# Kernel optimization log

Hardware: AMD Instinct MI355X
Metric: run time of the kernel (lower is better)

Reference implementation:

```python
import jax, jax.numpy as jnp
from jax import lax
import numpy as np

B, T = 32, 15
THR1, THR2 = 15.0, 10.0  # conv1_t, conv2_t


def _conv(x, w):
    # x: (B,T,C,H,W) cumulative potentials/spikes; conv applied per timestep
    b, t, c, h, wd = x.shape
    y = lax.conv_general_dilated(x.reshape(b * t, c, h, wd), w, (1, 1), 'VALID',
                                 dimension_numbers=('NCHW', 'OIHW', 'NCHW'))
    return y.reshape(b, t, *y.shape[1:])


def _pool(x, k, s):
    b, t, c, h, wd = x.shape
    y = lax.reduce_window(x.reshape(b * t, c, h, wd), -jnp.inf, lax.max,
                          (1, 1, k, k), (1, 1, s, s), 'VALID')
    return y.reshape(b, t, *y.shape[1:])


def _pad(x, p):
    return jnp.pad(x, ((0, 0), (0, 0), (0, 0), (p, p), (p, p)))


def _fire(pot, thr):
    # sf.fire: F.threshold_(pot, thr, 0); spk = sign
    th = jnp.where(pot > thr, pot, 0.0)
    return jnp.sign(th), th


def _winner_class(pot, spk):
    # sf.get_k_winners(pot, kwta=1, r=0, spk): earliest spike, tie-break by potential
    b, t = spk.shape[:2]
    cnt = spk.sum(axis=1)                                   # (B,F,H,W) spike counts
    first = jnp.clip((t - cnt).astype(jnp.int32), 0, t - 1)  # earliest spike time
    vals = jnp.take_along_axis(pot, first[:, None], axis=1)[:, 0]  # pot at spike time
    trunc = spk * vals[:, None]                              # (B,T,F,H,W)
    v = trunc.reshape(b, -1).max(axis=1) * t                 # dominance offset per sample
    total = (trunc + spk * v[:, None, None, None, None]).sum(axis=1)  # (B,F,H,W)
    flat = total.reshape(b, -1)
    idx = jnp.argmax(flat, axis=1)
    mx = jnp.max(flat, axis=1)
    hw = pot.shape[-1] * pot.shape[-2]
    feat = idx // hw
    # decision_map: 10 classes x 20 features each -> class = feat // 20; -1 if no spike
    return jnp.where(mx != 0, feat // 20, -1).astype(jnp.int32)


def setup_inputs() -> dict:
    key = jax.random.key(0)
    k1, k2, k3, k4 = jax.random.split(key, 4)
    # cumulative binary spike wave: neuron fires at t_fire and stays 1 afterwards
    t_fire = jax.random.randint(k1, (B, 18, 32, 32), 0, T + 1)
    inp = (jnp.arange(T)[None, :, None, None, None] >= t_fire[:, None]).astype(jnp.float32)
    w1 = 0.8 + 0.05 * jax.random.normal(k2, (90, 18, 7, 7), dtype=jnp.float32)
    w2 = 0.8 + 0.05 * jax.random.normal(k3, (250, 90, 5, 5), dtype=jnp.float32)
    w3 = 0.8 + 0.05 * jax.random.normal(k4, (200, 250, 5, 5), dtype=jnp.float32)
    return {'input': inp, 'w1': w1, 'w2': w2, 'w3': w3, 'max_layer': 3}


def reference(input, w1, w2, w3, max_layer):
    # eval-mode forward of CIFAR10Net
    x = _pad(input, 2)                       # (B,T,18,36,36)
    spk1, pot1 = _fire(_conv(x, w1), THR1)   # (B,T,90,30,30)
    if max_layer == 1:
        return spk1, pot1
    spk2, pot2 = _fire(_conv(_pad(_pool(spk1, 2, 2), 1), w2), THR2)  # (B,T,250,13,13)
    if max_layer == 2:
        return spk2, pot2
    pot3 = _conv(_pad(_pool(spk2, 3, 3), 2), w3)   # (B,T,200,4,4)
    t = pot3.shape[1]
    mask = (jnp.arange(t) == t - 1).astype(pot3.dtype)[None, :, None, None, None]
    spk3 = jnp.sign(pot3 * mask)             # fire with threshold=None: only last step
    cls = _winner_class(pot3, spk3)          # (B,) predicted class or -1
    return cls, pot3
```

## Files before the change

kernel.cpp:

```cpp
#include <hip/hip_runtime.h>

#define NB 32
#define NT 15


__device__ __forceinline__ void tr_tile(const float* __restrict__ src, float* __restrict__ dst,
                                        int F, int K, int KK, int CIN, int nkt, int t, int tid) {
    __shared__ float lds[32][33];
    int kt = t % nkt, ft = t / nkt;
    int k0 = kt * 32, f0 = ft * 32;
    int tx = tid & 31, ty = tid >> 5;
#pragma unroll
    for (int i = 0; i < 4; i++) {
        int fl = ty + 8 * i;
        int f = f0 + fl, k = k0 + tx;
        lds[fl][tx] = (f < F && k < K) ? src[(size_t)f * K + k] : 0.f;
    }
    __syncthreads();
#pragma unroll
    for (int i = 0; i < 4; i++) {
        int row = ty + 8 * i;
        int k = k0 + row, f = f0 + tx;
        if (k < K && f < F) {
            int j = (k % KK) * CIN + k / KK;
            dst[(size_t)j * F + f] = lds[tx][row];
        }
    }
}

__global__ __launch_bounds__(256) void k_pre1(const float* __restrict__ inp,
                                              const float* __restrict__ w1,
                                              const float* __restrict__ w2,
                                              const float* __restrict__ w3,
                                              unsigned char* __restrict__ ft0,
                                              float* __restrict__ wT1, float* __restrict__ wT2,
                                              float* __restrict__ wT3,
                                              float* __restrict__ Pmin1) {
    int blk = blockIdx.x, tid = threadIdx.x;
    if (blk < 972) {
        int idx = blk * 256 + tid;
        int xx = idx % 36, rest = idx / 36;
        int yy = rest % 36; rest /= 36;
        int g = rest % 6;  int b = rest / 6;
        unsigned char* dst = ft0 + ((size_t)(b * 36 + yy) * 36 + xx) * 18 + g * 3;
        int x = xx - 2, y = yy - 2;
        if (x >= 0 && x < 32 && y >= 0 && y < 32) {
            int c0 = 0, c1 = 0, c2 = 0;
            const float* p = inp + ((size_t)b * NT * 18 + g * 3) * 1024 + y * 32 + x;
#pragma unroll
            for (int t = 0; t < NT; t++) {
                c0 += (p[(size_t)(t * 18 + 0) * 1024] != 0.f);
                c1 += (p[(size_t)(t * 18 + 1) * 1024] != 0.f);
                c2 += (p[(size_t)(t * 18 + 2) * 1024] != 0.f);
            }
            dst[0] = (unsigned char)(15 - c0);
            dst[1] = (unsigned char)(15 - c1);
            dst[2] = (unsigned char)(15 - c2);
        } else {
            dst[0] = 15; dst[1] = 15; dst[2] = 15;
        }
    } else if (blk < 2996) {
        const float* src; float* dst;
        int F, K, KK, CIN, nkt, t;
        if (blk < 1056)      { src = w1; dst = wT1; F = 90;  K = 882;  KK = 49; CIN = 18;  nkt = 28;  t = blk - 972; }
        else if (blk < 1624) { src = w2; dst = wT2; F = 250; K = 2250; KK = 25; CIN = 90;  nkt = 71;  t = blk - 1056; }
        else                 { src = w3; dst = wT3; F = 200; K = 6250; KK = 25; CIN = 250; nkt = 196; t = blk - 1624; }
        tr_tile(src, dst, F, K, KK, CIN, nkt, t, tid);
    } else if (blk == 2996) {
        if (tid < 90)  wT1[882 * 90 + tid] = 0.f;
        if (tid < 250) wT2[(size_t)2250 * 250 + tid] = 0.f;
        if (tid < 200) wT3[(size_t)6250 * 200 + tid] = 0.f;
    } else {
        int bb = blk - 2997;
        __shared__ float wm[4];
        float m = 1e30f;
#pragma unroll
        for (int k = 0; k < 8; k++) {
            int i = bb * 2048 + k * 256 + tid;
            if (i < 90 * 882) m = fminf(m, w1[i]);
        }
        for (int o = 32; o > 0; o >>= 1) m = fminf(m, __shfl_down(m, o));
        if ((tid & 63) == 0) wm[tid >> 6] = m;
        __syncthreads();
        if (tid == 0) Pmin1[bb] = fminf(fminf(wm[0], wm[1]), fminf(wm[2], wm[3]));
    }
}

__global__ __launch_bounds__(256) void k_pre2(const unsigned char* __restrict__ ft0,
                                              const float* __restrict__ wT2,
                                              const float* __restrict__ wT3,
                                              const float* __restrict__ Pmin1,
                                              unsigned char* __restrict__ zmap,
                                              float* __restrict__ PosS2, float* __restrict__ PosS3,
                                              float* __restrict__ m1) {
    int blk = blockIdx.x, tid = threadIdx.x;
    if (blk < 162) {
        int idx = blk * 256 + tid;
        const unsigned char* p = ft0 + (size_t)idx * 18;
        int z = 0;
#pragma unroll
        for (int c = 0; c < 18; c++) z += (p[c] == 0);
        zmap[idx] = (unsigned char)z;
    } else if (blk < 187) {
        int pos = blk - 162;
        int f = tid < 250 ? tid : 249;
        float acc = 0.f;
        for (int c = 0; c < 90; c++) acc += wT2[(size_t)(pos * 90 + c) * 250 + f];
        if (tid < 250) PosS2[pos * 256 + tid] = acc;
    } else if (blk < 212) {
        int pos = blk - 187;
        int f = tid < 200 ? tid : 199;
        float acc = 0.f;
        for (int c = 0; c < 250; c++) acc += wT3[(size_t)(pos * 250 + c) * 200 + f];
        if (tid < 200) PosS3[pos * 200 + tid] = acc;
    } else {
        if (tid < 64) {
            float m = (tid < 40) ? Pmin1[tid] : 1e30f;
            for (int o = 32; o > 0; o >>= 1) m = fminf(m, __shfl_down(m, o));
            if (tid == 0) m1[0] = m;
        }
    }
}

__global__ __launch_bounds__(256) void k_pre3(const float* __restrict__ PosS2,
                                              const float* __restrict__ PosS3,
                                              float* __restrict__ W2e, float* __restrict__ W3s) {
    int b = blockIdx.x, tid = threadIdx.x;
    if (b < 169) {
        int f = tid < 250 ? tid : 249;
        int oy = b / 13, ox = b - oy * 13;
        float s = 0.f;
#pragma unroll
        for (int pos = 0; pos < 25; pos++) {
            int r = pos / 5, x = pos - r * 5;
            int gy = oy + r, gx = ox + x;
            if (!(gy == 0 || gy == 16 || gx == 0 || gx == 16)) s += PosS2[pos * 256 + f];
        }
        if (tid < 250) W2e[b * 256 + tid] = s;
    } else {
        int px = b - 169;
        int f = tid < 200 ? tid : 199;
        int oy = px >> 2, ox = px & 3;
        int r0 = max(0, 2 - oy), r1 = min(4, 5 - oy);
        int x0 = max(0, 2 - ox), x1 = min(4, 5 - ox);
        float s = 0.f;
        for (int r = r0; r <= r1; r++)
            for (int x = x0; x <= x1; x++)
                s += PosS3[(r * 5 + x) * 200 + f];
        if (tid < 200) W3s[px * 200 + tid] = s;
    }
}

__global__ __launch_bounds__(128) void k_conv1f(const unsigned char* __restrict__ ft0,
                                                const unsigned char* __restrict__ zmap,
                                                const float* __restrict__ wT1,
                                                const float* __restrict__ m1p,
                                                unsigned char* __restrict__ ft1) {
    __shared__ __align__(16) int list[896];
    __shared__ int cnt, pcnt, cnt0s;
    int tid = threadIdx.x;
    int px = blockIdx.x, b = blockIdx.y;
    int oy = px / 30, ox = px - oy * 30;
    int zv = 0;
    if (tid < 49) zv = zmap[(b * 36 + oy + tid / 7) * 36 + ox + tid % 7];
    if (tid < 64) {
        for (int o = 32; o > 0; o >>= 1) zv += __shfl_down(zv, o);
        if (tid == 0) cnt0s = zv;
    }
    __syncthreads();
    if ((float)cnt0s * m1p[0] > 15.0f) {
        if (tid < 90) ft1[((size_t)(b * 30 + oy) * 30 + ox) * 90 + tid] = 0;
        return;
    }
    const unsigned char* base = ft0 + ((size_t)(b * 36 + oy) * 36 + ox) * 18;
    unsigned char myft[7];
#pragma unroll
    for (int k = 0; k < 7; k++) {
        int j = tid + k * 128;
        if (j < 882) {
            int r = j / 126;
            myft[k] = base[j + 522 * r];
        } else myft[k] = 255;
    }
    int f = tid < 90 ? tid : 89;
    const char* wb = (const char*)(wT1 + f);
    const int zoff = 882 * 90 * 4;
    float acc = 0.f; int ft = 15;
    for (int s = 0; s < 15; s++) {
        if (tid == 0) cnt = 0;
        __syncthreads();
#pragma unroll
        for (int k = 0; k < 7; k++) {
            if ((int)myft[k] == s) { int p = atomicAdd(&cnt, 1); list[p] = (tid + k * 128) * 360; }
        }
        __syncthreads();
        if (tid == 0) {
            int c0 = cnt, cp = (c0 + 7) & ~7;
            for (int i = c0; i < cp; i++) list[i] = zoff;
            pcnt = cp;
        }
        __syncthreads();
        int e = pcnt;
        for (int i = 0; i < e; i += 8) {
            int4 p0 = *(const int4*)(list + i);
            int4 p1 = *(const int4*)(list + i + 4);
            int o0 = __builtin_amdgcn_readfirstlane(p0.x);
            int o1 = __builtin_amdgcn_readfirstlane(p0.y);
            int o2 = __builtin_amdgcn_readfirstlane(p0.z);
            int o3 = __builtin_amdgcn_readfirstlane(p0.w);
            int o4 = __builtin_amdgcn_readfirstlane(p1.x);
            int o5 = __builtin_amdgcn_readfirstlane(p1.y);
            int o6 = __builtin_amdgcn_readfirstlane(p1.z);
            int o7 = __builtin_amdgcn_readfirstlane(p1.w);
            float a0 = *(const float*)(wb + o0);
            float a1 = *(const float*)(wb + o1);
            float a2 = *(const float*)(wb + o2);
            float a3 = *(const float*)(wb + o3);
            float a4 = *(const float*)(wb + o4);
            float a5 = *(const float*)(wb + o5);
            float a6 = *(const float*)(wb + o6);
            float a7 = *(const float*)(wb + o7);
            acc += ((a0 + a1) + (a2 + a3)) + ((a4 + a5) + (a6 + a7));
        }
        if (ft == 15 && acc > 15.0f) ft = s;
        if (__syncthreads_and(ft != 15)) break;
    }
    if (tid < 90) ft1[((size_t)(b * 30 + oy) * 30 + ox) * 90 + tid] = (unsigned char)ft;
}

__global__ __launch_bounds__(256) void k_conv2cr(const unsigned char* __restrict__ ft1p,
                                                 const float* __restrict__ wT2,
                                                 const float* __restrict__ W2e,
                                                 unsigned char* __restrict__ ft2) {
    constexpr int PADCAP = 2250 + 15 * 8;
    __shared__ __align__(16) int perm[PADCAP];
    __shared__ int start[16], cur[16];
    __shared__ int cntCs;
    int tid = threadIdx.x;
    int px = blockIdx.x, b = blockIdx.y;
    int oy = px / 13, ox = px - oy * 13;
    const unsigned char* base = ft1p + ((size_t)(b * 17 + oy) * 17 + ox) * 90;
    if (tid == 0) cntCs = 0;
    if (tid < 16) cur[tid] = 0;
    unsigned char myft[9];
    int nc = 0;
#pragma unroll
    for (int k = 0; k < 9; k++) {
        int j = tid + k * 256;
        myft[k] = 0;
        if (j < 2250) {
            int r = j / 450;
            myft[k] = base[j + 1080 * r];
        }
        nc += (myft[k] >= 1);
    }
    for (int o = 32; o > 0; o >>= 1) nc += __shfl_down(nc, o);
    __syncthreads();
    if ((tid & 63) == 0) atomicAdd(&cntCs, nc);
    __syncthreads();
    int f = tid < 250 ? tid : 249;
    float W = W2e[px * 256 + f];
    if (cntCs == 0) {
        if (tid < 250) ft2[((size_t)(b * 13 + oy) * 13 + ox) * 250 + tid] = (W > 10.0f) ? 0 : 15;
        return;
    }
#pragma unroll
    for (int k = 0; k < 9; k++) { int v = myft[k]; if (v >= 1) atomicAdd(&cur[v - 1], 1); }
    __syncthreads();
    if (tid == 0) {
        int s = 0;
#pragma unroll
        for (int j = 0; j < 15; j++) { int c = cur[j]; start[j] = s; s += (c + 7) & ~7; }
        start[15] = s;
    }
    __syncthreads();
    int nnzp = start[15];
    if (tid < 15) cur[tid] = start[tid];
    const int zoff = 2250 * 250 * 4;
    for (int i = tid; i < nnzp; i += 256) perm[i] = zoff;
    __syncthreads();
#pragma unroll
    for (int k = 0; k < 9; k++) {
        int v = myft[k];
        if (v >= 1) { int p = atomicAdd(&cur[v - 1], 1); perm[p] = (tid + k * 256) * 1000; }
    }
    __syncthreads();
    const char* wb = (const char*)(wT2 + f);
    float R = 0.f; int ft = 15;
    for (int j = 14; j >= 0; j--) {
        int sjb = start[j], e = start[j + 1];
        for (int i = sjb; i < e; i += 8) {
            int4 p0 = *(const int4*)(perm + i);
            int4 p1 = *(const int4*)(perm + i + 4);
            int o0 = __builtin_amdgcn_readfirstlane(p0.x);
            int o1 = __builtin_amdgcn_readfirstlane(p0.y);
            int o2 = __builtin_amdgcn_readfirstlane(p0.z);
            int o3 = __builtin_amdgcn_readfirstlane(p0.w);
            int o4 = __builtin_amdgcn_readfirstlane(p1.x);
            int o5 = __builtin_amdgcn_readfirstlane(p1.y);
            int o6 = __builtin_amdgcn_readfirstlane(p1.z);
            int o7 = __builtin_amdgcn_readfirstlane(p1.w);
            float a0 = *(const float*)(wb + o0);
            float a1 = *(const float*)(wb + o1);
            float a2 = *(const float*)(wb + o2);
            float a3 = *(const float*)(wb + o3);
            float a4 = *(const float*)(wb + o4);
            float a5 = *(const float*)(wb + o5);
            float a6 = *(const float*)(wb + o6);
            float a7 = *(const float*)(wb + o7);
            R += ((a0 + a1) + (a2 + a3)) + ((a4 + a5) + (a6 + a7));
        }
        float pot = W - R;
        if (pot > 10.0f) ft = j;
        if (sjb == 0) { if (pot > 10.0f) ft = 0; break; }
        if (__all(pot <= 10.0f)) break;
    }
    if (tid < 250) ft2[((size_t)(b * 13 + oy) * 13 + ox) * 250 + tid] = (unsigned char)ft;
}

__global__ __launch_bounds__(256) void k_conv3cr(const unsigned char* __restrict__ ft2p,
                                                 const float* __restrict__ wT3,
                                                 const float* __restrict__ W3s,
                                                 float* __restrict__ out) {
    constexpr int PADCAP = 4000 + 15 * 8;
    __shared__ __align__(16) int perm[PADCAP];
    __shared__ int start[16], cur[16];
    __shared__ int offs[16], rowb[16];
    int tid = threadIdx.x;
    int px = blockIdx.x, b = blockIdx.y;
    int oy = px >> 2, ox = px & 3;
    int r0 = max(0, 2 - oy), r1 = min(4, 5 - oy);
    int x0 = max(0, 2 - ox), x1 = min(4, 5 - ox);
    int VR = r1 - r0 + 1, VC = x1 - x0 + 1;
    int NP = VR * VC, NV = NP * 250;
    if (tid < NP) {
        int rv = tid / VC, xv = tid - rv * VC;
        offs[tid] = ((r0 + rv) * 8 + (x0 + xv)) * 250;
        rowb[tid] = ((r0 + rv) * 5 + (x0 + xv)) * 250;
    }
    if (tid < 16) cur[tid] = 0;
    const unsigned char* base = ft2p + ((size_t)(b * 8 + oy) * 8 + ox) * 250;
    __syncthreads();
    unsigned char myft[16];
#pragma unroll
    for (int k = 0; k < 16; k++) {
        int i = tid + k * 256;
        myft[k] = 0;
        if (i < NV) {
            int posv = i / 250, c = i - posv * 250;
            myft[k] = base[offs[posv] + c];
        }
    }
#pragma unroll
    for (int k = 0; k < 16; k++) { int v = myft[k]; if (v >= 1) atomicAdd(&cur[v - 1], 1); }
    __syncthreads();
    if (tid == 0) {
        int s = 0;
#pragma unroll
        for (int j = 0; j < 15; j++) { int c = cur[j]; start[j] = s; s += (c + 7) & ~7; }
        start[15] = s;
    }
    __syncthreads();
    int nnzp = start[15];
    if (tid < 15) cur[tid] = start[tid];
    const int zoff = 6250 * 200 * 4;
    for (int i = tid; i < nnzp; i += 256) perm[i] = zoff;
    __syncthreads();
#pragma unroll
    for (int k = 0; k < 16; k++) {
        int v = myft[k];
        if (v >= 1) {
            int i = tid + k * 256;
            int posv = i / 250, c = i - posv * 250;
            int p = atomicAdd(&cur[v - 1], 1);
            perm[p] = (rowb[posv] + c) * 800;
        }
    }
    __syncthreads();

    int f = tid < 200 ? tid : 199;
    const char* wb = (const char*)(wT3 + f);
    float W = W3s[px * 200 + f];
    float* o = out + 32 + ((size_t)b * NT) * 3200 + f * 16 + px;
    float R = 0.f;
    for (int j = 14; j >= 0; j--) {
        int sjb = start[j], e = start[j + 1];
        for (int i = sjb; i < e; i += 8) {
            int4 p0 = *(const int4*)(perm + i);
            int4 p1 = *(const int4*)(perm + i + 4);
            int o0 = __builtin_amdgcn_readfirstlane(p0.x);
            int o1 = __builtin_amdgcn_readfirstlane(p0.y);
            int o2 = __builtin_amdgcn_readfirstlane(p0.z);
            int o3 = __builtin_amdgcn_readfirstlane(p0.w);
            int o4 = __builtin_amdgcn_readfirstlane(p1.x);
            int o5 = __builtin_amdgcn_readfirstlane(p1.y);
            int o6 = __builtin_amdgcn_readfirstlane(p1.z);
            int o7 = __builtin_amdgcn_readfirstlane(p1.w);
            float a0 = *(const float*)(wb + o0);
            float a1 = *(const float*)(wb + o1);
            float a2 = *(const float*)(wb + o2);
            float a3 = *(const float*)(wb + o3);
            float a4 = *(const float*)(wb + o4);
            float a5 = *(const float*)(wb + o5);
            float a6 = *(const float*)(wb + o6);
            float a7 = *(const float*)(wb + o7);
            R += ((a0 + a1) + (a2 + a3)) + ((a4 + a5) + (a6 + a7));
        }
        float pot = W - R;
        if (tid < 200) o[(size_t)j * 3200] = pot;
        if (sjb == 0) {
            for (int jj = j - 1; jj >= 0; jj--)
                if (tid < 200) o[(size_t)jj * 3200] = pot;
            break;
        }
    }
}

__global__ __launch_bounds__(256) void k_pool1c(const unsigned char* __restrict__ ft1,
                                                unsigned char* __restrict__ ft1p) {
    int idx = blockIdx.x * 256 + threadIdx.x;
    if (idx >= NB * 17 * 17 * 90) return;
    int c = idx % 90, rest = idx / 90;
    int xx = rest % 17; rest /= 17;
    int yy = rest % 17; int b = rest / 17;
    int ft = 0;
    if (xx >= 1 && xx < 16 && yy >= 1 && yy < 16) {
        const unsigned char* p = ft1 + ((size_t)(b * 30 + (yy - 1) * 2) * 30 + (xx - 1) * 2) * 90 + c;
        int m = p[0];
        m = min(m, (int)p[90]);
        m = min(m, (int)p[30 * 90]);
        m = min(m, (int)p[31 * 90]);
        ft = m;
    }
    ft1p[idx] = (unsigned char)ft;
}

__global__ __launch_bounds__(256) void k_pool2c(const unsigned char* __restrict__ ft2,
                                                unsigned char* __restrict__ ft2p) {
    int idx = blockIdx.x * 256 + threadIdx.x;
    if (idx >= NB * 8 * 8 * 250) return;
    int c = idx % 250, rest = idx / 250;
    int xx = rest % 8; rest /= 8;
    int yy = rest % 8; int b = rest / 8;
    int ft = 15;
    if (xx >= 2 && xx < 6 && yy >= 2 && yy < 6) {
        const unsigned char* p = ft2 + ((size_t)(b * 13 + (yy - 2) * 3) * 13 + (xx - 2) * 3) * 250 + c;
        int m = 15;
#pragma unroll
        for (int dy = 0; dy < 3; dy++)
#pragma unroll
            for (int dx = 0; dx < 3; dx++) m = min(m, (int)p[(dy * 13 + dx) * 250]);
        ft = m;
    }
    ft2p[idx] = (unsigned char)ft;
}

__global__ __launch_bounds__(256) void k_winner(const float* __restrict__ outp,
                                                float* __restrict__ outc) {
    int b = blockIdx.x, tid = threadIdx.x;
    const float* p14 = outp + 32 + ((size_t)b * NT + 14) * 3200;
    __shared__ float sv[256];
    __shared__ int   si[256];
    float m = 0.f;
    for (int j = tid; j < 3200; j += 256) {
        float v = p14[j];
        if (v > 0.f && v > m) m = v;
    }
    sv[tid] = m;
    __syncthreads();
    for (int s = 128; s > 0; s >>= 1) {
        if (tid < s) sv[tid] = fmaxf(sv[tid], sv[tid + s]);
        __syncthreads();
    }
    float vofs = 15.f * sv[0];
    __syncthreads();
    float bestv = 0.f; int besti = 0x3fffffff;
    for (int j = tid; j < 3200; j += 256) {
        float v = p14[j];
        float tot = (v > 0.f) ? v + vofs : 0.f;
        if (tot > bestv) { bestv = tot; besti = j; }
    }
    sv[tid] = bestv; si[tid] = besti;
    __syncthreads();
    for (int s = 128; s > 0; s >>= 1) {
        if (tid < s) {
            if (sv[tid + s] > sv[tid] || (sv[tid + s] == sv[tid] && si[tid + s] < si[tid])) {
                sv[tid] = sv[tid + s]; si[tid] = si[tid + s];
            }
        }
        __syncthreads();
    }
    if (tid == 0) {
        float mx = sv[0];
        int cls = (mx != 0.f) ? ((si[0] / 16) / 20) : -1;
        outc[b] = (float)cls;
    }
}

extern "C" void kernel_launch(void* const* d_in, const int* in_sizes, int n_in,
                              void* d_out, int out_size, void* d_ws, size_t ws_size,
                              hipStream_t stream) {
    const float* inp = (const float*)d_in[0];
    const float* w1  = (const float*)d_in[1];
    const float* w2  = (const float*)d_in[2];
    const float* w3  = (const float*)d_in[3];
    float* out = (float*)d_out;

    unsigned char* ws   = (unsigned char*)d_ws;
    unsigned char* ft0  = ws;
    unsigned char* ft1  = ws + 746496;
    unsigned char* ft1p = ws + 3338496;
    unsigned char* ft2  = ws + 4170816;
    unsigned char* ft2p = ws + 5522816;
    float* wT1   = (float*)(ws + 6034816);
    float* wT2   = (float*)(ws + 6352704);
    float* wT3   = (float*)(ws + 8603712);
    float* W3s   = (float*)(ws + 13605568);
    float* PosS2 = (float*)(ws + 13618368);
    float* W2e   = (float*)(ws + 13643968);
    float* Pmin1 = (float*)(ws + 13817024);
    float* m1    = (float*)(ws + 13817280);
    unsigned char* zmap = ws + 13817344;
    float* PosS3 = (float*)(ws + 13858816);

    hipLaunchKernelGGL(k_pre1, dim3(3037), dim3(256), 0, stream,
                       inp, w1, w2, w3, ft0, wT1, wT2, wT3, Pmin1);
    hipLaunchKernelGGL(k_pre2, dim3(213), dim3(256), 0, stream,
                       ft0, wT2, wT3, Pmin1, zmap, PosS2, PosS3, m1);
    hipLaunchKernelGGL(k_pre3, dim3(185), dim3(256), 0, stream, PosS2, PosS3, W2e, W3s);

    hipLaunchKernelGGL(k_conv1f, dim3(900, NB), dim3(128), 0, stream, ft0, zmap, wT1, m1, ft1);
    hipLaunchKernelGGL(k_pool1c, dim3((NB * 17 * 17 * 90 + 255) / 256), dim3(256), 0, stream, ft1, ft1p);
    hipLaunchKernelGGL(k_conv2cr, dim3(169, NB), dim3(256), 0, stream, ft1p, wT2, W2e, ft2);
    hipLaunchKernelGGL(k_pool2c, dim3((NB * 8 * 8 * 250 + 255) / 256), dim3(256), 0, stream, ft2, ft2p);
    hipLaunchKernelGGL(k_conv3cr, dim3(16, NB), dim3(256), 0, stream, ft2p, wT3, W3s, out);
    hipLaunchKernelGGL(k_winner, dim3(NB), dim3(256), 0, stream, out, out);
}
```

Measured before the change: 161.6 us.

## Fuse pooling into conv2/conv3 gathers and move zmap computation into k_pre1

Result: slower. 172.3 us (+6.6%).

```diff
diff --git a/kernel.cpp b/kernel.cpp
--- a/kernel.cpp
+++ b/kernel.cpp
@@ -33,6 +33,7 @@
                                               const float* __restrict__ w2,
                                               const float* __restrict__ w3,
                                               unsigned char* __restrict__ ft0,
+                                              unsigned char* __restrict__ zmap,
                                               float* __restrict__ wT1, float* __restrict__ wT2,
                                               float* __restrict__ wT3,
                                               float* __restrict__ Pmin1) {
@@ -59,19 +60,31 @@
         } else {
             dst[0] = 15; dst[1] = 15; dst[2] = 15;
         }
-    } else if (blk < 2996) {
+    } else if (blk < 1134) {
+        int idx = (blk - 972) * 256 + tid;
+        int xx = idx % 36, rest = idx / 36;
+        int yy = rest % 36; int b = rest / 36;
+        int x = xx - 2, y = yy - 2;
+        int z = 0;
+        if (x >= 0 && x < 32 && y >= 0 && y < 32) {
+            const float* p = inp + (size_t)b * NT * 18 * 1024 + y * 32 + x;
+#pragma unroll
+            for (int c = 0; c < 18; c++) z += (p[(size_t)c * 1024] != 0.f);
+        }
+        zmap[idx] = (unsigned char)z;
+    } else if (blk < 3158) {
         const float* src; float* dst;
         int F, K, KK, CIN, nkt, t;
-        if (blk < 1056)      { src = w1; dst = wT1; F = 90;  K = 882;  KK = 49; CIN = 18;  nkt = 28;  t = blk - 972; }
-        else if (blk < 1624) { src = w2; dst = wT2; F = 250; K = 2250; KK = 25; CIN = 90;  nkt = 71;  t = blk - 1056; }
-        else                 { src = w3; dst = wT3; F = 200; K = 6250; KK = 25; CIN = 250; nkt = 196; t = blk - 1624; }
+        if (blk < 1218)      { src = w1; dst = wT1; F = 90;  K = 882;  KK = 49; CIN = 18;  nkt = 28;  t = blk - 1134; }
+        else if (blk < 1786) { src = w2; dst = wT2; F = 250; K = 2250; KK = 25; CIN = 90;  nkt = 71;  t = blk - 1218; }
+        else                 { src = w3; dst = wT3; F = 200; K = 6250; KK = 25; CIN = 250; nkt = 196; t = blk - 1786; }
         tr_tile(src, dst, F, K, KK, CIN, nkt, t, tid);
-    } else if (blk == 2996) {
+    } else if (blk == 3158) {
         if (tid < 90)  wT1[882 * 90 + tid] = 0.f;
         if (tid < 250) wT2[(size_t)2250 * 250 + tid] = 0.f;
         if (tid < 200) wT3[(size_t)6250 * 200 + tid] = 0.f;
     } else {
-        int bb = blk - 2997;
+        int bb = blk - 3159;
         __shared__ float wm[4];
         float m = 1e30f;
 #pragma unroll
@@ -86,29 +99,20 @@
     }
 }
 
-__global__ __launch_bounds__(256) void k_pre2(const unsigned char* __restrict__ ft0,
-                                              const float* __restrict__ wT2,
+__global__ __launch_bounds__(256) void k_pre2(const float* __restrict__ wT2,
                                               const float* __restrict__ wT3,
                                               const float* __restrict__ Pmin1,
-                                              unsigned char* __restrict__ zmap,
                                               float* __restrict__ PosS2, float* __restrict__ PosS3,
                                               float* __restrict__ m1) {
     int blk = blockIdx.x, tid = threadIdx.x;
-    if (blk < 162) {
-        int idx = blk * 256 + tid;
-        const unsigned char* p = ft0 + (size_t)idx * 18;
-        int z = 0;
-#pragma unroll
-        for (int c = 0; c < 18; c++) z += (p[c] == 0);
-        zmap[idx] = (unsigned char)z;
-    } else if (blk < 187) {
-        int pos = blk - 162;
+    if (blk < 25) {
+        int pos = blk;
         int f = tid < 250 ? tid : 249;
         float acc = 0.f;
         for (int c = 0; c < 90; c++) acc += wT2[(size_t)(pos * 90 + c) * 250 + f];
         if (tid < 250) PosS2[pos * 256 + tid] = acc;
-    } else if (blk < 212) {
-        int pos = blk - 187;
+    } else if (blk < 50) {
+        int pos = blk - 25;
         int f = tid < 200 ? tid : 199;
         float acc = 0.f;
         for (int c = 0; c < 250; c++) acc += wT3[(size_t)(pos * 250 + c) * 200 + f];
@@ -228,7 +232,7 @@
     if (tid < 90) ft1[((size_t)(b * 30 + oy) * 30 + ox) * 90 + tid] = (unsigned char)ft;
 }
 
-__global__ __launch_bounds__(256) void k_conv2cr(const unsigned char* __restrict__ ft1p,
+__global__ __launch_bounds__(256) void k_conv2cr(const unsigned char* __restrict__ ft1,
                                                  const float* __restrict__ wT2,
                                                  const float* __restrict__ W2e,
                                                  unsigned char* __restrict__ ft2) {
@@ -239,7 +243,7 @@
     int tid = threadIdx.x;
     int px = blockIdx.x, b = blockIdx.y;
     int oy = px / 13, ox = px - oy * 13;
-    const unsigned char* base = ft1p + ((size_t)(b * 17 + oy) * 17 + ox) * 90;
+    const unsigned char* fb = ft1 + (size_t)b * 900 * 90;
     if (tid == 0) cntCs = 0;
     if (tid < 16) cur[tid] = 0;
     unsigned char myft[9];
@@ -249,8 +253,17 @@
         int j = tid + k * 256;
         myft[k] = 0;
         if (j < 2250) {
-            int r = j / 450;
-            myft[k] = base[j + 1080 * r];
+            int c = j % 90, pos = j / 90;
+            int r = pos / 5, x = pos - r * 5;
+            int gy = oy + r, gx = ox + x;
+            if (gy >= 1 && gy <= 15 && gx >= 1 && gx <= 15) {
+                const unsigned char* q = fb + ((size_t)((gy - 1) * 2) * 30 + (gx - 1) * 2) * 90 + c;
+                int m = q[0];
+                m = min(m, (int)q[90]);
+                m = min(m, (int)q[2700]);
+                m = min(m, (int)q[2790]);
+                myft[k] = (unsigned char)m;
+            }
         }
         nc += (myft[k] >= 1);
     }
@@ -318,7 +331,7 @@
     if (tid < 250) ft2[((size_t)(b * 13 + oy) * 13 + ox) * 250 + tid] = (unsigned char)ft;
 }
 
-__global__ __launch_bounds__(256) void k_conv3cr(const unsigned char* __restrict__ ft2p,
+__global__ __launch_bounds__(256) void k_conv3cr(const unsigned char* __restrict__ ft2,
                                                  const float* __restrict__ wT3,
                                                  const float* __restrict__ W3s,
                                                  float* __restrict__ out) {
@@ -335,11 +348,12 @@
     int NP = VR * VC, NV = NP * 250;
     if (tid < NP) {
         int rv = tid / VC, xv = tid - rv * VC;
-        offs[tid] = ((r0 + rv) * 8 + (x0 + xv)) * 250;
+        int py = oy + r0 + rv, gx = ox + x0 + xv;
+        offs[tid] = (((py - 2) * 3) * 13 + (gx - 2) * 3) * 250;
         rowb[tid] = ((r0 + rv) * 5 + (x0 + xv)) * 250;
     }
     if (tid < 16) cur[tid] = 0;
-    const unsigned char* base = ft2p + ((size_t)(b * 8 + oy) * 8 + ox) * 250;
+    const unsigned char* base2 = ft2 + (size_t)b * 169 * 250;
     __syncthreads();
     unsigned char myft[16];
 #pragma unroll
@@ -348,7 +362,12 @@
         myft[k] = 0;
         if (i < NV) {
             int posv = i / 250, c = i - posv * 250;
-            myft[k] = base[offs[posv] + c];
+            const unsigned char* q = base2 + offs[posv] + c;
+            int m = q[0];
+            m = min(m, (int)q[250]);  m = min(m, (int)q[500]);
+            m = min(m, (int)q[3250]); m = min(m, (int)q[3500]); m = min(m, (int)q[3750]);
+            m = min(m, (int)q[6500]); m = min(m, (int)q[6750]); m = min(m, (int)q[7000]);
+            myft[k] = (unsigned char)m;
         }
     }
 #pragma unroll
@@ -416,45 +435,6 @@
     }
 }
 
-__global__ __launch_bounds__(256) void k_pool1c(const unsigned char* __restrict__ ft1,
-                                                unsigned char* __restrict__ ft1p) {
-    int idx = blockIdx.x * 256 + threadIdx.x;
-    if (idx >= NB * 17 * 17 * 90) return;
-    int c = idx % 90, rest = idx / 90;
-    int xx = rest % 17; rest /= 17;
-    int yy = rest % 17; int b = rest / 17;
-    int ft = 0;
-    if (xx >= 1 && xx < 16 && yy >= 1 && yy < 16) {
-        const unsigned char* p = ft1 + ((size_t)(b * 30 + (yy - 1) * 2) * 30 + (xx - 1) * 2) * 90 + c;
-        int m = p[0];
-        m = min(m, (int)p[90]);
-        m = min(m, (int)p[30 * 90]);
-        m = min(m, (int)p[31 * 90]);
-        ft = m;
-    }
-    ft1p[idx] = (unsigned char)ft;
-}
-
-__global__ __launch_bounds__(256) void k_pool2c(const unsigned char* __restrict__ ft2,
-                                                unsigned char* __restrict__ ft2p) {
-    int idx = blockIdx.x * 256 + threadIdx.x;
-    if (idx >= NB * 8 * 8 * 250) return;
-    int c = idx % 250, rest = idx / 250;
-    int xx = rest % 8; rest /= 8;
-    int yy = rest % 8; int b = rest / 8;
-    int ft = 15;
-    if (xx >= 2 && xx < 6 && yy >= 2 && yy < 6) {
-        const unsigned char* p = ft2 + ((size_t)(b * 13 + (yy - 2) * 3) * 13 + (xx - 2) * 3) * 250 + c;
-        int m = 15;
-#pragma unroll
-        for (int dy = 0; dy < 3; dy++)
-#pragma unroll
-            for (int dx = 0; dx < 3; dx++) m = min(m, (int)p[(dy * 13 + dx) * 250]);
-        ft = m;
-    }
-    ft2p[idx] = (unsigned char)ft;
-}
-
 __global__ __launch_bounds__(256) void k_winner(const float* __restrict__ outp,
                                                 float* __restrict__ outc) {
     int b = blockIdx.x, tid = threadIdx.x;
@@ -509,9 +489,7 @@
     unsigned char* ws   = (unsigned char*)d_ws;
     unsigned char* ft0  = ws;
     unsigned char* ft1  = ws + 746496;
-    unsigned char* ft1p = ws + 3338496;
     unsigned char* ft2  = ws + 4170816;
-    unsigned char* ft2p = ws + 5522816;
     float* wT1   = (float*)(ws + 6034816);
     float* wT2   = (float*)(ws + 6352704);
     float* wT3   = (float*)(ws + 8603712);
@@ -523,16 +501,13 @@
     unsigned char* zmap = ws + 13817344;
     float* PosS3 = (float*)(ws + 13858816);
 
-    hipLaunchKernelGGL(k_pre1, dim3(3037), dim3(256), 0, stream,
-                       inp, w1, w2, w3, ft0, wT1, wT2, wT3, Pmin1);
-    hipLaunchKernelGGL(k_pre2, dim3(213), dim3(256), 0, stream,
-                       ft0, wT2, wT3, Pmin1, zmap, PosS2, PosS3, m1);
+    hipLaunchKernelGGL(k_pre1, dim3(3199), dim3(256), 0, stream,
+                       inp, w1, w2, w3, ft0, zmap, wT1, wT2, wT3, Pmin1);
+    hipLaunchKernelGGL(k_pre2, dim3(51), dim3(256), 0, stream, wT2, wT3, Pmin1, PosS2, PosS3, m1);
     hipLaunchKernelGGL(k_pre3, dim3(185), dim3(256), 0, stream, PosS2, PosS3, W2e, W3s);
 
     hipLaunchKernelGGL(k_conv1f, dim3(900, NB), dim3(128), 0, stream, ft0, zmap, wT1, m1, ft1);
-    hipLaunchKernelGGL(k_pool1c, dim3((NB * 17 * 17 * 90 + 255) / 256), dim3(256), 0, stream, ft1, ft1p);
-    hipLaunchKernelGGL(k_conv2cr, dim3(169, NB), dim3(256), 0, stream, ft1p, wT2, W2e, ft2);
-    hipLaunchKernelGGL(k_pool2c, dim3((NB * 8 * 8 * 250 + 255) / 256), dim3(256), 0, stream, ft2, ft2p);
-    hipLaunchKernelGGL(k_conv3cr, dim3(16, NB), dim3(256), 0, stream, ft2p, wT3, W3s, out);
+    hipLaunchKernelGGL(k_conv2cr, dim3(169, NB), dim3(256), 0, stream, ft1, wT2, W2e, ft2);
+    hipLaunchKernelGGL(k_conv3cr, dim3(16, NB), dim3(256), 0, stream, ft2, wT3, W3s, out);
     hipLaunchKernelGGL(k_winner, dim3(NB), dim3(256), 0, stream, out, out);
 }
```
